# Performance work log

Hardware: AMD Instinct MI355X
Metric: run time of the kernel (lower is better)

## Reference

```python
import jax, jax.numpy as jnp
import numpy as np

T, B, E, H = 2048, 2, 1024, 16
Dh = E // H


def setup_inputs() -> dict:
    key = jax.random.key(0)
    ks = jax.random.split(key, 5)
    s = 0.02
    query = jax.random.normal(ks[0], (T, B, E), dtype=jnp.float32)
    Wq = jax.random.normal(ks[1], (E, E), dtype=jnp.float32) * s
    Wk = jax.random.normal(ks[2], (E, E), dtype=jnp.float32) * s
    Wv = jax.random.normal(ks[3], (E, E), dtype=jnp.float32) * s
    Wo = jax.random.normal(ks[4], (E, E), dtype=jnp.float32) * s
    bq = jnp.zeros((E,), jnp.float32)
    bk = jnp.zeros((E,), jnp.float32)
    bv = jnp.zeros((E,), jnp.float32)
    bo = jnp.zeros((E,), jnp.float32)
    # additive causal mask: 0 on/below diagonal, -inf above (standard fairseq usage)
    neg = jnp.finfo(jnp.float32).min
    attn_mask = jnp.where(jnp.triu(jnp.ones((T, T), jnp.bool_), k=1), neg, 0.0).astype(jnp.float32)
    return {"query": query, "Wq": Wq, "bq": bq, "Wk": Wk, "bk": bk,
            "Wv": Wv, "bv": bv, "Wo": Wo, "bo": bo, "attn_mask": attn_mask}


def reference(query, Wq, bq, Wk, bk, Wv, bv, Wo, bo, attn_mask):
    t, b, e = query.shape
    scale = Dh ** -0.5
    # self-attention projections (nn.Linear: x @ W.T + b)
    q = (query @ Wq.T + bq) * scale  # [T,B,E]
    k = query @ Wk.T + bk
    v = query @ Wv.T + bv
    # [T, B*H, Dh] -> [B*H, T, Dh]
    q = q.reshape(t, b * H, Dh).transpose(1, 0, 2)
    k = k.reshape(t, b * H, Dh).transpose(1, 0, 2)
    v = v.reshape(t, b * H, Dh).transpose(1, 0, 2)
    # explicit bmm -> softmax -> bmm (materializes [B*H, T, T])
    attn_weights = jnp.einsum('btd,bsd->bts', q, k) + attn_mask[None, :, :]
    attn_probs = jax.nn.softmax(attn_weights, axis=-1)
    attn = jnp.einsum('bts,bsd->btd', attn_probs, v)  # [B*H, T, Dh]
    attn = attn.transpose(1, 0, 2).reshape(t, b, e)  # [T,B,E]
    out = attn @ Wo.T + bo
    return out
```

## Files before the change

### kernel.cpp

```cpp
#include <hip/hip_runtime.h>


typedef __attribute__((ext_vector_type(8))) short   s16x8;
typedef __attribute__((ext_vector_type(4))) float   f32x4;
typedef __attribute__((ext_vector_type(2))) __fp16  f16x2;
typedef __attribute__((ext_vector_type(4))) __fp16  f16x4;

#define MFMA16(a, b, c) __builtin_amdgcn_mfma_f32_16x16x32_bf16((a), (b), (c), 0, 0, 0)
#define MFMApv(a, b, c) __builtin_amdgcn_mfma_f32_16x16x16f16((a), (b), (c), 0, 0, 0)

static __device__ __forceinline__ unsigned short f2bf(float f) {
    unsigned u = __float_as_uint(f);
    unsigned r = u + 0x7fffu + ((u >> 16) & 1u);
    return (unsigned short)(r >> 16);
}

static __device__ __forceinline__ void gl2lds16(const void* g, void* l) {
    __builtin_amdgcn_global_load_lds(
        (const __attribute__((address_space(1))) unsigned int*)g,
        (__attribute__((address_space(3))) unsigned int*)l, 16, 0, 0);
}

__global__ __launch_bounds__(256) void cvt_all(const float* __restrict__ query,
                                               const float* __restrict__ w0,
                                               const float* __restrict__ w1,
                                               const float* __restrict__ w2,
                                               const float* __restrict__ w3,
                                               unsigned short* __restrict__ Xb,
                                               unsigned short* __restrict__ Wcat) {
    const int bx = blockIdx.x;
    if (bx < 4096) {
        const int i = threadIdx.x;
        const float4 f = reinterpret_cast<const float4*>(query + (size_t)bx * 1024)[i];
        ushort4 u;
        u.x = f2bf(f.x); u.y = f2bf(f.y); u.z = f2bf(f.z); u.w = f2bf(f.w);
        const int mrow = (bx & 1) * 2048 + (bx >> 1);
        reinterpret_cast<ushort4*>(Xb + (size_t)mrow * 1024)[i] = u;
    } else {
        const int j   = bx - 4096;
        const int sel = j >> 10;
        const int i   = (j & 1023) * 256 + threadIdx.x;
        const float* src = (sel == 0) ? w0 : (sel == 1) ? w1 : (sel == 2) ? w2 : w3;
        const float4 f = reinterpret_cast<const float4*>(src)[i];
        ushort4 u;
        u.x = f2bf(f.x); u.y = f2bf(f.y); u.z = f2bf(f.z); u.w = f2bf(f.w);
        reinterpret_cast<ushort4*>(Wcat + (size_t)sel * 1048576)[i] = u;
    }
}

__global__ __launch_bounds__(512, 2) void gemm_qkv(const unsigned short* __restrict__ A,
                                                   const unsigned short* __restrict__ W,
                                                   const float* __restrict__ b0,
                                                   const float* __restrict__ b1,
                                                   const float* __restrict__ b2,
                                                   unsigned short* __restrict__ outQK,
                                                   __fp16* __restrict__ outV) {
    __shared__ __align__(16) unsigned short smem[65536];

    const int tid  = threadIdx.x;
    const int w    = tid >> 6;
    const int lane = tid & 63;
    const int quad = lane >> 4;
    const int c    = lane & 15;
    const int wm   = w >> 2;
    const int wn   = w & 3;

    const int id   = blockIdx.x;
    const int xcd  = id & 7;
    const int slot = id >> 3;
    const int m0 = (xcd * 2 + (slot & 1)) * 256;
    const int n0 = (slot >> 1) * 256;

    f32x4 acc[8][4];
    #pragma unroll
    for (int mi = 0; mi < 8; ++mi)
        #pragma unroll
        for (int ni = 0; ni < 4; ++ni) acc[mi][ni] = (f32x4){0.f, 0.f, 0.f, 0.f};

    const int srow = tid >> 3;
    const int g    = (tid & 7) ^ (srow & 7);
    const unsigned short* aG = A + (size_t)(m0 + srow) * 1024 + g * 8;
    const unsigned short* wG = W + (size_t)(n0 + srow) * 1024 + g * 8;
    const int loff = tid * 8;

#define STA(buf, u, k0) gl2lds16(aG + (k0) + (u) * 65536, &smem[(buf) * 32768 + (u) * 4096 + loff])
#define STB(buf, u, k0) gl2lds16(wG + (k0) + (u) * 65536, &smem[(buf) * 32768 + 16384 + (u) * 4096 + loff])

    STB(0, 0, 0); STB(0, 1, 0); STB(0, 2, 0); STB(0, 3, 0);
    STA(0, 0, 0); STA(0, 2, 0); STA(0, 1, 0); STA(0, 3, 0);
    asm volatile("s_waitcnt vmcnt(2)" ::: "memory");
    asm volatile("s_barrier" ::: "memory");

    const int cs  = c & 7;
    const int ch0 = (quad ^ cs) << 3;
    const int ch1 = ((4 + quad) ^ cs) << 3;

    s16x8 af[4][2], bl[2][2], bh[2][2];

    #pragma unroll 1
    for (int t = 0; t < 16; ++t) {
        const unsigned short* Al = &smem[(t & 1) * 32768];
        const unsigned short* Bl = Al + 16384;
        const int  nb   = (t & 1) ^ 1;
        const int  kn   = (t + 1) * 64;
        const bool more = (t < 15);

        #pragma unroll
        for (int mi = 0; mi < 4; ++mi) {
            const int row = (wm * 128 + mi * 16 + c) * 64;
            af[mi][0] = *reinterpret_cast<const s16x8*>(&Al[row + ch0]);
            af[mi][1] = *reinterpret_cast<const s16x8*>(&Al[row + ch1]);
        }
        #pragma unroll
        for (int ni = 0; ni < 2; ++ni) {
            const int row = (wn * 64 + ni * 16 + c) * 64;
            bl[ni][0] = *reinterpret_cast<const s16x8*>(&Bl[row + ch0]);
            bl[ni][1] = *reinterpret_cast<const s16x8*>(&Bl[row + ch1]);
        }
        if (more) { STB(nb, 0, kn); STB(nb, 1, kn); }
        asm volatile("s_barrier" ::: "memory");
        __builtin_amdgcn_s_setprio(1);
        #pragma unroll
        for (int mi = 0; mi < 4; ++mi)
            #pragma unroll
            for (int ni = 0; ni < 2; ++ni) {
                acc[mi][ni] = MFMA16(af[mi][0], bl[ni][0], acc[mi][ni]);
                acc[mi][ni] = MFMA16(af[mi][1], bl[ni][1], acc[mi][ni]);
            }
        __builtin_amdgcn_s_setprio(0);
        asm volatile("s_barrier" ::: "memory");

        #pragma unroll
        for (int ni = 0; ni < 2; ++ni) {
            const int row = (wn * 64 + (2 + ni) * 16 + c) * 64;
            bh[ni][0] = *reinterpret_cast<const s16x8*>(&Bl[row + ch0]);
            bh[ni][1] = *reinterpret_cast<const s16x8*>(&Bl[row + ch1]);
        }
        if (more) { STB(nb, 2, kn); STB(nb, 3, kn); }
        asm volatile("s_barrier" ::: "memory");
        __builtin_amdgcn_s_setprio(1);
        #pragma unroll
        for (int mi = 0; mi < 4; ++mi)
            #pragma unroll
            for (int ni = 0; ni < 2; ++ni) {
                acc[mi][2 + ni] = MFMA16(af[mi][0], bh[ni][0], acc[mi][2 + ni]);
                acc[mi][2 + ni] = MFMA16(af[mi][1], bh[ni][1], acc[mi][2 + ni]);
            }
        __builtin_amdgcn_s_setprio(0);
        if (more) asm volatile("s_waitcnt vmcnt(4)" ::: "memory");
        else      asm volatile("s_waitcnt vmcnt(0)" ::: "memory");
        asm volatile("s_barrier" ::: "memory");

        #pragma unroll
        for (int mi = 0; mi < 4; ++mi) {
            const int row = (wm * 128 + (4 + mi) * 16 + c) * 64;
            af[mi][0] = *reinterpret_cast<const s16x8*>(&Al[row + ch0]);
            af[mi][1] = *reinterpret_cast<const s16x8*>(&Al[row + ch1]);
        }
        if (more) { STA(nb, 0, kn); STA(nb, 2, kn); }
        asm volatile("s_barrier" ::: "memory");
        __builtin_amdgcn_s_setprio(1);
        #pragma unroll
        for (int mi = 0; mi < 4; ++mi)
            #pragma unroll
            for (int ni = 0; ni < 2; ++ni) {
                acc[4 + mi][ni] = MFMA16(af[mi][0], bl[ni][0], acc[4 + mi][ni]);
                acc[4 + mi][ni] = MFMA16(af[mi][1], bl[ni][1], acc[4 + mi][ni]);
            }
        __builtin_amdgcn_s_setprio(0);
        asm volatile("s_barrier" ::: "memory");

        if (more) { STA(nb, 1, kn); STA(nb, 3, kn); }
        asm volatile("s_barrier" ::: "memory");
        __builtin_amdgcn_s_setprio(1);
        #pragma unroll
        for (int mi = 0; mi < 4; ++mi)
            #pragma unroll
            for (int ni = 0; ni < 2; ++ni) {
                acc[4 + mi][2 + ni] = MFMA16(af[mi][0], bh[ni][0], acc[4 + mi][2 + ni]);
                acc[4 + mi][2 + ni] = MFMA16(af[mi][1], bh[ni][1], acc[4 + mi][2 + ni]);
            }
        __builtin_amdgcn_s_setprio(0);
        if (more) asm volatile("s_waitcnt vmcnt(2)" ::: "memory");
        asm volatile("s_barrier" ::: "memory");
    }
#undef STA
#undef STB

    if (n0 < 2048) {
        const float scale = (n0 < 1024) ? 0.18033688011112042f : 1.0f;
        const float* bias = (n0 < 1024) ? b0 : b1;
        #pragma unroll
        for (int ni = 0; ni < 4; ++ni) {
            const int n = n0 + wn * 64 + ni * 16 + c;
            const float bval = bias[n & 1023];
            #pragma unroll
            for (int mi = 0; mi < 8; ++mi)
                #pragma unroll
                for (int r = 0; r < 4; ++r) {
                    const int m = m0 + wm * 128 + mi * 16 + quad * 4 + r;
                    outQK[(size_t)m * 2048 + n] = f2bf((acc[mi][ni][r] + bval) * scale);
                }
        }
    } else {
        __fp16* lds16 = reinterpret_cast<__fp16*>(smem);
        #pragma unroll 1
        for (int tn = 0; tn < 2; ++tn) {
            __syncthreads();
            if ((wn >> 1) == tn) {
                #pragma unroll
                for (int ni = 0; ni < 4; ++ni) {
                    const int nLoc = (wn & 1) * 64 + ni * 16 + c;
                    const float bval = b2[(n0 - 2048) + tn * 128 + nLoc];
                    #pragma unroll
                    for (int mi = 0; mi < 8; ++mi) {
                        const int mLoc = mi * 16 + quad * 4;
                        const f16x2 lo = __builtin_amdgcn_cvt_pkrtz(acc[mi][ni][0] + bval,
                                                                    acc[mi][ni][1] + bval);
                        const f16x2 hi = __builtin_amdgcn_cvt_pkrtz(acc[mi][ni][2] + bval,
                                                                    acc[mi][ni][3] + bval);
                        uint2 st;
                        st.x = __builtin_bit_cast(unsigned int, lo);
                        st.y = __builtin_bit_cast(unsigned int, hi);
                        const int phys = wm * 16384 + nLoc * 128 +
                                         (((mLoc >> 3) ^ (nLoc & 15)) << 3) + (mLoc & 7);
                        *reinterpret_cast<uint2*>(&lds16[phys]) = st;
                    }
                }
            }
            __syncthreads();
            const int np   = tid >> 1;
            const int rg   = np >> 7;
            const int nLoc = np & 127;
            const int vcol = (n0 - 2048) + tn * 128 + nLoc;
            const int bb = m0 >> 11;
            const int tbase = (m0 & 2047) + rg * 128;
            __fp16* vdst = outV + ((size_t)((bb * 16 + (vcol >> 6)) * 64 + (vcol & 63))) * 2048 + tbase;
            #pragma unroll
            for (int j = 0; j < 8; ++j) {
                const int lc = (tid & 1) * 8 + j;
                *reinterpret_cast<uint4*>(vdst + lc * 8) =
                    *reinterpret_cast<const uint4*>(
                        &lds16[rg * 16384 + nLoc * 128 + ((lc ^ (nLoc & 15)) << 3)]);
            }
        }
    }
}

__global__ __launch_bounds__(256) void gemm_out(const unsigned short* __restrict__ A,
                                                const unsigned short* __restrict__ W,
                                                const float* __restrict__ bias,
                                                float* __restrict__ outF) {
    __shared__ __align__(16) unsigned short Al[64 * 64];
    __shared__ __align__(16) unsigned short Bl[128 * 64];

    const int tid  = threadIdx.x;
    const int w    = tid >> 6;
    const int lane = tid & 63;
    const int quad = lane >> 4;
    const int c    = lane & 15;

    const int id   = blockIdx.x;
    const int xcd  = id & 7;
    const int slot = id >> 3;
    const int m0 = (xcd * 8 + (slot & 7)) * 64;
    const int n0 = (slot >> 3) * 128;

    f32x4 acc[8];
    #pragma unroll
    for (int ni = 0; ni < 8; ++ni) acc[ni] = (f32x4){0.f, 0.f, 0.f, 0.f};

    const int srow = tid >> 3;
    const int g    = (tid & 7) ^ (srow & 7);
    const unsigned short* aG = A + (size_t)(m0 + srow) * 1024 + g * 8;
    const unsigned short* wG = W + (size_t)(n0 + srow) * 1024 + g * 8;
    const int loff = tid * 8;

    const int cs = (c & 7);

    for (int kk = 0; kk < 16; ++kk) {
        const int k0 = kk * 64;
        __syncthreads();
        gl2lds16(aG + k0,             &Al[loff]);
        gl2lds16(aG + k0 + 32 * 1024, &Al[loff + 2048]);
        #pragma unroll
        for (int i = 0; i < 4; ++i)
            gl2lds16(wG + k0 + i * 32 * 1024, &Bl[loff + i * 2048]);
        __syncthreads();

        const int arow = (w * 16 + c) * 64;
        const s16x8 af0 = *reinterpret_cast<const s16x8*>(&Al[arow + ((quad ^ cs) << 3)]);
        const s16x8 af1 = *reinterpret_cast<const s16x8*>(&Al[arow + (((4 + quad) ^ cs) << 3)]);
        #pragma unroll
        for (int ni = 0; ni < 8; ++ni) {
            const int brow = (ni * 16 + c) * 64;
            const s16x8 bf0 = *reinterpret_cast<const s16x8*>(&Bl[brow + ((quad ^ cs) << 3)]);
            const s16x8 bf1 = *reinterpret_cast<const s16x8*>(&Bl[brow + (((4 + quad) ^ cs) << 3)]);
            acc[ni] = MFMA16(af0, bf0, acc[ni]);
            acc[ni] = MFMA16(af1, bf1, acc[ni]);
        }
    }

    #pragma unroll
    for (int ni = 0; ni < 8; ++ni) {
        const int n = n0 + ni * 16 + c;
        const float bval = bias[n];
        const int m = m0 + w * 16 + quad * 4;
        const int bb = m >> 11, t = m & 2047;
        #pragma unroll
        for (int r = 0; r < 4; ++r)
            outF[(size_t)(2 * (t + r) + bb) * 1024 + n] = acc[ni][r] + bval;
    }
}

__global__ __launch_bounds__(256, 4) void attn_kernel(const unsigned short* __restrict__ QKb,
                                                      const __fp16* __restrict__ Vt,
                                                      unsigned short* __restrict__ Ob) {
    __shared__ unsigned short Kl[2][2][64][32];
    __shared__ __fp16 Vl[2][64][64];

    const int tid  = threadIdx.x;
    const int w    = tid >> 6;
    const int lane = tid & 63;
    const int quad = lane >> 4;
    const int c    = lane & 15;

    const int id = blockIdx.x;
    const int bh = (id & 7) * 4 + ((id >> 3) & 3);
    const int a  = 31 - (id >> 5);
    const int bB = bh >> 4, h = bh & 15;
    const int t0 = a * 64;
    const int trg = t0 + w * 16;
    const int nIt = a + 1;

    const unsigned short* qp = QKb + (size_t)(bB * 2048 + trg + c) * 2048 + h * 64 + quad * 8;
    const s16x8 aq0 = *reinterpret_cast<const s16x8*>(qp);
    const s16x8 aq1 = *reinterpret_cast<const s16x8*>(qp + 32);

    const int lr4 = lane >> 2, sl4 = lane & 3;
    const unsigned short* kSrc = QKb + (size_t)(bB * 2048 + w * 16 + lr4) * 2048
                                 + 1024 + h * 64 + (sl4 ^ ((lane >> 3) & 3)) * 8;
    const int vr8 = lane >> 3, sl8 = lane & 7;
    const __fp16* vSrcA = Vt + (size_t)(bh * 64 + w * 16 + vr8) * 2048 + (sl8 ^ vr8) * 8;
    const __fp16* vSrcB = vSrcA + (size_t)8 * 2048;

    f32x4 acc[4];
    float l = 0.f;
    #pragma unroll
    for (int dt = 0; dt < 4; ++dt) acc[dt] = (f32x4){0.f, 0.f, 0.f, 0.f};

    const int kswz = (quad ^ ((c >> 1) & 3)) * 8;

    {
        gl2lds16(kSrc,      &Kl[0][0][w * 16 + lr4][sl4 * 8]);
        gl2lds16(kSrc + 32, &Kl[0][1][w * 16 + lr4][sl4 * 8]);
        gl2lds16(vSrcA,     &Vl[0][w * 16 + vr8][sl8 * 8]);
        gl2lds16(vSrcB,     &Vl[0][w * 16 + 8 + vr8][sl8 * 8]);
    }

    for (int it = 0; it < nIt; ++it) {
        const int buf = it & 1;
        __syncthreads();
        if (it + 1 < nIt) {
            const size_t s1 = (size_t)(it + 1) * 64;
            const int nb = buf ^ 1;
            gl2lds16(kSrc + s1 * 2048,      &Kl[nb][0][w * 16 + lr4][sl4 * 8]);
            gl2lds16(kSrc + s1 * 2048 + 32, &Kl[nb][1][w * 16 + lr4][sl4 * 8]);
            gl2lds16(vSrcA + s1,            &Vl[nb][w * 16 + vr8][sl8 * 8]);
            gl2lds16(vSrcB + s1,            &Vl[nb][w * 16 + 8 + vr8][sl8 * 8]);
        }

        s16x8 kf[4][2];
        #pragma unroll
        for (int ns = 0; ns < 4; ++ns) {
            kf[ns][0] = *reinterpret_cast<const s16x8*>(&Kl[buf][0][ns * 16 + c][kswz]);
            kf[ns][1] = *reinterpret_cast<const s16x8*>(&Kl[buf][1][ns * 16 + c][kswz]);
        }
        f16x4 vf[4][4];
        #pragma unroll
        for (int dt = 0; dt < 4; ++dt)
            #pragma unroll
            for (int ch = 0; ch < 4; ++ch) {
                const int phys = ((2 * ch + (quad >> 1)) ^ (c & 7)) * 8 + (quad & 1) * 4;
                vf[dt][ch] = *reinterpret_cast<const f16x4*>(&Vl[buf][dt * 16 + c][phys]);
            }

        const int s0 = it * 64;
        const bool diag = (it == a);
        f32x4 sT[4];
        #pragma unroll
        for (int ns = 0; ns < 4; ++ns) {
            f32x4 z = (f32x4){0.f, 0.f, 0.f, 0.f};
            z = MFMA16(kf[ns][0], aq0, z);
            sT[ns] = MFMA16(kf[ns][1], aq1, z);
        }
        f16x4 pf[4];
        float lp = 0.f;
        #pragma unroll
        for (int ns = 0; ns < 4; ++ns) {
            float pv[4];
            #pragma unroll
            for (int r = 0; r < 4; ++r) pv[r] = exp2f(sT[ns][r]);
            if (diag) {
                const int sb = s0 + ns * 16 + quad * 4;
                const int qg = trg + c;
                #pragma unroll
                for (int r = 0; r < 4; ++r) if (sb + r > qg) pv[r] = 0.f;
            }
            lp += (pv[0] + pv[1]) + (pv[2] + pv[3]);
            const f16x2 lo = __builtin_amdgcn_cvt_pkrtz(pv[0], pv[1]);
            const f16x2 hi = __builtin_amdgcn_cvt_pkrtz(pv[2], pv[3]);
            pf[ns] = __builtin_shufflevector(lo, hi, 0, 1, 2, 3);
        }
        l += lp;
        #pragma unroll
        for (int dt = 0; dt < 4; ++dt)
            #pragma unroll
            for (int ns = 0; ns < 4; ++ns)
                acc[dt] = MFMApv(vf[dt][ns], pf[ns], acc[dt]);
    }

    float lv = l;
    lv += __shfl_xor(lv, 16);
    lv += __shfl_xor(lv, 32);
    const float inv = 1.0f / lv;
    const size_t base = (size_t)(bB * 2048 + trg + c) * 1024 + h * 64;
    #pragma unroll
    for (int dt = 0; dt < 4; ++dt) {
        const unsigned u0 = (unsigned)f2bf(acc[dt][0] * inv)
                          | ((unsigned)f2bf(acc[dt][1] * inv) << 16);
        const unsigned u1 = (unsigned)f2bf(acc[dt][2] * inv)
                          | ((unsigned)f2bf(acc[dt][3] * inv) << 16);
        uint2 st; st.x = u0; st.y = u1;
        *reinterpret_cast<uint2*>(Ob + base + dt * 16 + quad * 4) = st;
    }
}

extern "C" void kernel_launch(void* const* d_in, const int* in_sizes, int n_in,
                              void* d_out, int out_size, void* d_ws, size_t ws_size,
                              hipStream_t stream) {
    const float* query = (const float*)d_in[0];
    const float* Wq    = (const float*)d_in[1];
    const float* bq    = (const float*)d_in[2];
    const float* Wk    = (const float*)d_in[3];
    const float* bk    = (const float*)d_in[4];
    const float* Wv    = (const float*)d_in[5];
    const float* bv    = (const float*)d_in[6];
    const float* Wo    = (const float*)d_in[7];
    const float* bo    = (const float*)d_in[8];

    float* out = (float*)d_out;

    unsigned short* ws    = (unsigned short*)d_ws;
    unsigned short* Xbf   = ws;
    unsigned short* Wcat  = Xbf  + (size_t)4096 * 1024;
    unsigned short* QKb   = Wcat + (size_t)4 * 1024 * 1024;
    __fp16*         Vtw   = (__fp16*)(QKb + (size_t)4096 * 2048);
    unsigned short* attnb = (unsigned short*)(Vtw + (size_t)32 * 64 * 2048);

    cvt_all<<<8192, 256, 0, stream>>>(query, Wq, Wk, Wv, Wo, Xbf, Wcat);

    gemm_qkv<<<192, 512, 0, stream>>>(Xbf, Wcat, bq, bk, bv, QKb, Vtw);

    attn_kernel<<<1024, 256, 0, stream>>>(QKb, Vtw, attnb);

    gemm_out<<<512, 256, 0, stream>>>(attnb, Wcat + (size_t)3 * 1024 * 1024,
                                      bo, out);
}
```

Before: 192.8 us.

## Double-buffer out-projection GEMM, reorder causal attention blocks, add setprio and raw exp2

The output-projection GEMM now double-buffers its LDS tiles, so the next K-slice loads while the current one feeds MFMAs, and one barrier per iteration is removed. The attention kernel maps block ids to query tiles in a serpentine order, balancing causal workload across waves of blocks. MFMA sections in both kernels are wrapped in s_setprio, and exp2f is replaced by the hardware exp2 builtin. Double-buffering doubles LDS use in gemm_out, which may lower occupancy, and the raw exp2 builtin may handle denormals or range differently.

```diff
diff --git a/kernel.cpp b/kernel.cpp
--- a/kernel.cpp
+++ b/kernel.cpp
@@ -251,8 +251,8 @@
                                                 const unsigned short* __restrict__ W,
                                                 const float* __restrict__ bias,
                                                 float* __restrict__ outF) {
-    __shared__ __align__(16) unsigned short Al[64 * 64];
-    __shared__ __align__(16) unsigned short Bl[128 * 64];
+    __shared__ __align__(16) unsigned short Al[2][64 * 64];
+    __shared__ __align__(16) unsigned short Bl[2][128 * 64];
 
     const int tid  = threadIdx.x;
     const int w    = tid >> 6;
@@ -278,27 +278,38 @@
 
     const int cs = (c & 7);
 
+    gl2lds16(aG,             &Al[0][loff]);
+    gl2lds16(aG + 32 * 1024, &Al[0][loff + 2048]);
+    #pragma unroll
+    for (int i = 0; i < 4; ++i)
+        gl2lds16(wG + i * 32 * 1024, &Bl[0][loff + i * 2048]);
+
+    #pragma unroll 1
     for (int kk = 0; kk < 16; ++kk) {
-        const int k0 = kk * 64;
         __syncthreads();
-        gl2lds16(aG + k0,             &Al[loff]);
-        gl2lds16(aG + k0 + 32 * 1024, &Al[loff + 2048]);
-        #pragma unroll
-        for (int i = 0; i < 4; ++i)
-            gl2lds16(wG + k0 + i * 32 * 1024, &Bl[loff + i * 2048]);
-        __syncthreads();
-
+        if (kk < 15) {
+            const int k0n = (kk + 1) * 64;
+            const int nb  = (kk + 1) & 1;
+            gl2lds16(aG + k0n,             &Al[nb][loff]);
+            gl2lds16(aG + k0n + 32 * 1024, &Al[nb][loff + 2048]);
+            #pragma unroll
+            for (int i = 0; i < 4; ++i)
+                gl2lds16(wG + k0n + i * 32 * 1024, &Bl[nb][loff + i * 2048]);
+        }
+        const int cb = kk & 1;
         const int arow = (w * 16 + c) * 64;
-        const s16x8 af0 = *reinterpret_cast<const s16x8*>(&Al[arow + ((quad ^ cs) << 3)]);
-        const s16x8 af1 = *reinterpret_cast<const s16x8*>(&Al[arow + (((4 + quad) ^ cs) << 3)]);
+        const s16x8 af0 = *reinterpret_cast<const s16x8*>(&Al[cb][arow + ((quad ^ cs) << 3)]);
+        const s16x8 af1 = *reinterpret_cast<const s16x8*>(&Al[cb][arow + (((4 + quad) ^ cs) << 3)]);
+        __builtin_amdgcn_s_setprio(1);
         #pragma unroll
         for (int ni = 0; ni < 8; ++ni) {
             const int brow = (ni * 16 + c) * 64;
-            const s16x8 bf0 = *reinterpret_cast<const s16x8*>(&Bl[brow + ((quad ^ cs) << 3)]);
-            const s16x8 bf1 = *reinterpret_cast<const s16x8*>(&Bl[brow + (((4 + quad) ^ cs) << 3)]);
+            const s16x8 bf0 = *reinterpret_cast<const s16x8*>(&Bl[cb][brow + ((quad ^ cs) << 3)]);
+            const s16x8 bf1 = *reinterpret_cast<const s16x8*>(&Bl[cb][brow + (((4 + quad) ^ cs) << 3)]);
             acc[ni] = MFMA16(af0, bf0, acc[ni]);
             acc[ni] = MFMA16(af1, bf1, acc[ni]);
         }
+        __builtin_amdgcn_s_setprio(0);
     }
 
     #pragma unroll
@@ -327,7 +338,9 @@
 
     const int id = blockIdx.x;
     const int bh = (id & 7) * 4 + ((id >> 3) & 3);
-    const int a  = 31 - (id >> 5);
+    const int kidx = id >> 5;
+    const int rr   = kidx >> 3, jj = kidx & 7;
+    const int a    = (rr & 1) ? (24 - 8 * rr + jj) : (31 - 8 * rr - jj);
     const int bB = bh >> 4, h = bh & 15;
     const int t0 = a * 64;
     const int trg = t0 + w * 16;
@@ -388,19 +401,21 @@
         const int s0 = it * 64;
         const bool diag = (it == a);
         f32x4 sT[4];
+        __builtin_amdgcn_s_setprio(1);
         #pragma unroll
         for (int ns = 0; ns < 4; ++ns) {
             f32x4 z = (f32x4){0.f, 0.f, 0.f, 0.f};
             z = MFMA16(kf[ns][0], aq0, z);
             sT[ns] = MFMA16(kf[ns][1], aq1, z);
         }
+        __builtin_amdgcn_s_setprio(0);
         f16x4 pf[4];
         float lp = 0.f;
         #pragma unroll
         for (int ns = 0; ns < 4; ++ns) {
             float pv[4];
             #pragma unroll
-            for (int r = 0; r < 4; ++r) pv[r] = exp2f(sT[ns][r]);
+            for (int r = 0; r < 4; ++r) pv[r] = __builtin_amdgcn_exp2f(sT[ns][r]);
             if (diag) {
                 const int sb = s0 + ns * 16 + quad * 4;
                 const int qg = trg + c;
@@ -413,11 +428,13 @@
             pf[ns] = __builtin_shufflevector(lo, hi, 0, 1, 2, 3);
         }
         l += lp;
+        __builtin_amdgcn_s_setprio(1);
         #pragma unroll
         for (int dt = 0; dt < 4; ++dt)
             #pragma unroll
             for (int ns = 0; ns < 4; ++ns)
                 acc[dt] = MFMApv(vf[dt][ns], pf[ns], acc[dt]);
+        __builtin_amdgcn_s_setprio(0);
     }
 
     float lv = l;
```

After: 195.6 us. About the same (+1.5%).
